# Performance work log

Measured on AMD Instinct MI355X. Metric: run time of the kernel, lower is better.

## Reference

```python
import jax, jax.numpy as jnp
import numpy as np
import math

B = 8192       # batch (tokens)
HID = 4096     # hidden size
H = 32         # num query heads
KV = 8         # num kv heads
GQA = H // KV  # 4
D = 128        # head dim
RBIT = 128     # hash bits
QKV = (H + 2 * KV) * D  # 6144


def setup_inputs() -> dict:
    key = jax.random.key(0)
    k1, k2, k3 = jax.random.split(key, 3)
    hidden = jax.random.normal(k1, (B, HID), jnp.float32)
    proj_w = jax.random.normal(k2, (HID, QKV), jnp.float32) * 0.02
    proj_b = jnp.zeros((QKV,), jnp.float32)
    # xavier_uniform init for hash weight [D, RBIT]
    limit = math.sqrt(6.0 / (D + RBIT))
    hash_w = jax.random.uniform(k3, (D, RBIT), jnp.float32, -limit, limit)
    return {"hidden": hidden, "proj_w": proj_w, "proj_b": proj_b, "hash_w": hash_w}


def reference(hidden, proj_w, proj_b, hash_w):
    # fused qkv projection
    qkv = hidden @ proj_w + proj_b                     # [B, QKV]
    q = qkv[:, : H * D].reshape(B, H, D)               # [B, H, D]
    k = qkv[:, H * D : (H + KV) * D].reshape(B, KV, 1, D)
    k = jnp.broadcast_to(k, (B, KV, GQA, D)).reshape(B, H, D)  # GQA expand

    inv_sqrt_d = 1.0 / math.sqrt(D)
    attn_weights = jnp.einsum("bhd,bhd->bh", q, k) * inv_sqrt_d  # with_norm=True

    # hash codes: BinaryStochastic (training mode): (tanh(x)+1)/2
    q_code = (jnp.tanh(q @ hash_w) + 1.0) * 0.5        # [B, H, RBIT]
    k_code = (jnp.tanh(k @ hash_w) + 1.0) * 0.5
    ham_dist = jnp.abs(q_code - k_code).sum(axis=-1)   # [B, H]
    ham_weights = 1.0 - 2.0 * ham_dist / RBIT

    # with_norm: scale by |q| |k| / sqrt(D)
    q_norm = jnp.linalg.norm(q, axis=-1)
    k_norm = jnp.linalg.norm(k, axis=-1)
    ham_weights = ham_weights * q_norm * k_norm * inv_sqrt_d

    return attn_weights.reshape(-1), ham_weights.reshape(-1)
```

## Files before the change

### kernel.cpp

```cpp
#include <hip/hip_runtime.h>
#include <hip/hip_bf16.h>
#include <cstdint>
#include <cstddef>

#define B_TOK 8192
#define HID   4096
#define NH    32
#define NKV   8
#define DH    128
#define RB    128
#define KDIM  4096
#define NOUT  5120
#define QKVW  6144

typedef __bf16 bf16x8 __attribute__((ext_vector_type(8)));
typedef __bf16 bf16x4 __attribute__((ext_vector_type(4)));
typedef float  f32x4  __attribute__((ext_vector_type(4)));

__device__ __forceinline__ void async_ld16(const void* g, void* l) {
  __builtin_amdgcn_global_load_lds(
      (__attribute__((address_space(1))) void*)(g),
      (__attribute__((address_space(3))) void*)(l), 16, 0, 0);
}

__device__ __forceinline__ float code_of(float x) {
  const float e = exp2f(x * -2.885390081777927f);
  return __builtin_amdgcn_rcpf(1.0f + e);
}


#define NB_HID  16384
#define NB_WT   5120
#define NB_HASH 64

__global__ void prep_kernel(const float* __restrict__ hidden, __bf16* __restrict__ Abf,
                            const float* __restrict__ W, __bf16* __restrict__ Wt,
                            const float* __restrict__ hw, __bf16* __restrict__ hwT) {
  __shared__ float t[64][65];
  const int bx  = blockIdx.x;
  const int tid = threadIdx.x;

  if (bx < NB_HID) {
    const int i = bx * 256 + tid;
    const float4 v0 = ((const float4*)hidden)[2 * i];
    const float4 v1 = ((const float4*)hidden)[2 * i + 1];
    bf16x8 o;
    o[0] = (__bf16)v0.x; o[1] = (__bf16)v0.y; o[2] = (__bf16)v0.z; o[3] = (__bf16)v0.w;
    o[4] = (__bf16)v1.x; o[5] = (__bf16)v1.y; o[6] = (__bf16)v1.z; o[7] = (__bf16)v1.w;
    ((bf16x8*)Abf)[i] = o;
  } else if (bx < NB_HID + NB_WT) {
    const int bt = bx - NB_HID;
    const int n0 = (bt % 80) * 64;
    const int k0 = (bt / 80) * 64;
    const int c4 = tid & 15;
    const int rr = tid >> 4;
#pragma unroll
    for (int j = 0; j < 4; ++j) {
      const int r = rr + j * 16;
      const float4 v = *(const float4*)&W[(size_t)(k0 + r) * QKVW + n0 + c4 * 4];
      t[r][c4 * 4 + 0] = v.x; t[r][c4 * 4 + 1] = v.y;
      t[r][c4 * 4 + 2] = v.z; t[r][c4 * 4 + 3] = v.w;
    }
    __syncthreads();
    const int c8 = tid & 7;
    const int nn = tid >> 3;
#pragma unroll
    for (int jj = 0; jj < 2; ++jj) {
      const int n = nn + jj * 32;
      bf16x8 o;
#pragma unroll
      for (int i = 0; i < 8; ++i) o[i] = (__bf16)t[c8 * 8 + i][n];
      *(bf16x8*)&Wt[(size_t)(n0 + n) * KDIM + k0 + c8 * 8] = o;
    }
  } else {
    const int idx = (bx - NB_HID - NB_WT) * 256 + tid;
    const int r = idx >> 7;
    const int d = idx & 127;
    hwT[r * RB + d] = (__bf16)hw[(size_t)d * RB + r];
  }
}


#define BK    32
#define KT    (KDIM / BK)
#define SLOT  24576

__global__ __launch_bounds__(256, 2) void gemm_qk(const __bf16* __restrict__ A,
                                                  const __bf16* __restrict__ Bt,
                                                  const float* __restrict__ bias,
                                                  __bf16* __restrict__ C) {
  __shared__ __align__(1024) char smem[3 * SLOT];

  const int tid  = threadIdx.x;
  const int lane = tid & 63;
  const int wave = tid >> 6;
  const int wm   = wave >> 1;
  const int wn   = wave & 1;

  const int lin = blockIdx.x;
  const int xcd = lin & 7;
  const int seq = lin >> 3;
  const int m0  = (xcd * 8 + (seq & 7)) * 128;
  const int n0  = (seq >> 3) * 256;

  const int srow = tid >> 2;
  const int sxk  = ((tid & 3) ^ ((tid >> 3) & 3)) * 8;
  const __bf16* ga = A  + (size_t)(m0 + srow) * KDIM + sxk;
  const __bf16* gb = Bt + (size_t)(n0 + srow) * KDIM + sxk;
  const int ldsA = wave * 1024;

#define STAGE(koff, sl) do {                                        \
    const __bf16* ga_ = ga + (koff);                                \
    const __bf16* gb_ = gb + (koff);                                \
    async_ld16(ga_,              (sl) + ldsA);                      \
    async_ld16(ga_ +  64 * KDIM, (sl) + 4096  + ldsA);              \
    async_ld16(gb_,              (sl) + 8192  + ldsA);              \
    async_ld16(gb_ +  64 * KDIM, (sl) + 12288 + ldsA);              \
    async_ld16(gb_ + 128 * KDIM, (sl) + 16384 + ldsA);              \
    async_ld16(gb_ + 192 * KDIM, (sl) + 20480 + ldsA);              \
  } while (0)

  const int fr = lane & 15;
  const int xc = (lane >> 4) ^ ((fr >> 1) & 3);
  const int aoff = (wm * 64 + fr) * 64 + xc * 16;
  const int boff = (wn * 128 + fr) * 64 + xc * 16;

  f32x4 acc[4][8] = {};

#define COMPUTE(sl) do {                                                          \
    bf16x8 af[4]; bf16x8 bfv[8];                                                  \
    _Pragma("unroll")                                                             \
    for (int mi = 0; mi < 4; ++mi)                                                \
      af[mi] = *(const bf16x8*)((sl) + aoff + mi * 1024);                         \
    _Pragma("unroll")                                                             \
    for (int ni = 0; ni < 8; ++ni)                                                \
      bfv[ni] = *(const bf16x8*)((sl) + 8192 + boff + ni * 1024);                 \
    __builtin_amdgcn_s_setprio(1);                                                \
    _Pragma("unroll")                                                             \
    for (int mi = 0; mi < 4; ++mi)                                                \
      _Pragma("unroll")                                                           \
      for (int ni = 0; ni < 8; ++ni)                                              \
        acc[mi][ni] = __builtin_amdgcn_mfma_f32_16x16x32_bf16(af[mi], bfv[ni],    \
                                                              acc[mi][ni], 0, 0, 0); \
    __builtin_amdgcn_s_setprio(0);                                                \
  } while (0)

  char* s0 = smem;
  char* s1 = smem + SLOT;
  char* s2 = smem + 2 * SLOT;

  STAGE(0, s0);
  STAGE(BK, s1);

  for (int t = 0; t < KT - 1; ++t) {
    asm volatile("s_waitcnt vmcnt(6)" ::: "memory");
    __builtin_amdgcn_s_barrier();
    __builtin_amdgcn_sched_barrier(0);
    if (t < KT - 2) STAGE((t + 2) * BK, s2);
    COMPUTE(s0);
    char* tmp = s0; s0 = s1; s1 = s2; s2 = tmp;
  }
  asm volatile("s_waitcnt vmcnt(0)" ::: "memory");
  __builtin_amdgcn_s_barrier();
  __builtin_amdgcn_sched_barrier(0);
  COMPUTE(s0);

#undef STAGE
#undef COMPUTE

  const int cl = lane & 15;
  const int rq = (lane >> 4) * 4;
#pragma unroll
  for (int ni = 0; ni < 8; ++ni) {
    const int gn = n0 + wn * 128 + ni * 16 + cl;
    const float bb = bias[gn];
#pragma unroll
    for (int mi = 0; mi < 4; ++mi) {
      const int gm = m0 + wm * 64 + mi * 16 + rq;
#pragma unroll
      for (int r = 0; r < 4; ++r)
        C[(size_t)(gm + r) * NOUT + gn] = (__bf16)(acc[mi][ni][r] + bb);
    }
  }
}


__global__ void phase2_kernel(const __bf16* __restrict__ QK,
                              const __bf16* __restrict__ hwT,
                              float* __restrict__ out) {
  __shared__ __bf16 As[48][136];
  __shared__ float code[40][132];
  __shared__ float rednorm[40];
  __shared__ float reddot[32];

  const int tid  = threadIdx.x;
  const int lane = tid & 63;
  const int wave = tid >> 6;
  const int b = blockIdx.x;

  const __bf16* src = QK + (size_t)b * NOUT;
  for (int i = tid; i < 640; i += 256) {
    const int row = i >> 4;
    const int col = (i & 15) * 8;
    *(uint4*)(&As[row][col]) = *(const uint4*)(src + i * 8);
  }

  const int fr = lane & 15;
  const int fk = (lane >> 4) * 8;
  bf16x8 bf[2][4];
#pragma unroll
  for (int nn = 0; nn < 2; ++nn) {
    const int ni = wave + nn * 4;
#pragma unroll
    for (int ks = 0; ks < 4; ++ks)
      bf[nn][ks] = *(const bf16x8*)(hwT + (size_t)(ni * 16 + fr) * RB + ks * 32 + fk);
  }
  __syncthreads();

#pragma unroll
  for (int mi = 0; mi < 3; ++mi) {
    bf16x8 af[4];
#pragma unroll
    for (int ks = 0; ks < 4; ++ks)
      af[ks] = *(const bf16x8*)(&As[mi * 16 + fr][ks * 32 + fk]);
#pragma unroll
    for (int nn = 0; nn < 2; ++nn) {
      const int ni = wave + nn * 4;
      f32x4 acc = {0.f, 0.f, 0.f, 0.f};
#pragma unroll
      for (int ks = 0; ks < 4; ++ks)
        acc = __builtin_amdgcn_mfma_f32_16x16x32_bf16(af[ks], bf[nn][ks], acc, 0, 0, 0);
      const int row0 = mi * 16 + (lane >> 4) * 4;
      const int col  = ni * 16 + (lane & 15);
#pragma unroll
      for (int r = 0; r < 4; ++r) {
        const int row = row0 + r;
        if (row < 40) code[row][col] = code_of(acc[r]);
      }
    }
  }

  {
    const int q = lane >> 4;
    const int c = lane & 15;
    const int ti = (wave == 1 || wave == 3) ? 1 : 0;
    const int tj = (wave >= 2) ? 2 : ti;
    bf16x8 fa[4], fb[4];
#pragma unroll
    for (int ks = 0; ks < 4; ++ks) {
      fa[ks] = *(const bf16x8*)(&As[ti * 16 + fr][ks * 32 + fk]);
      fb[ks] = *(const bf16x8*)(&As[tj * 16 + fr][ks * 32 + fk]);
    }
    f32x4 g = {0.f, 0.f, 0.f, 0.f};
#pragma unroll
    for (int ks = 0; ks < 4; ++ks)
      g = __builtin_amdgcn_mfma_f32_16x16x32_bf16(fa[ks], fb[ks], g, 0, 0, 0);
    if (ti == tj) {
      if ((c >> 2) == q) rednorm[ti * 16 + c] = g[c & 3];
    } else {
      if (c == ti * 4 + q) {
#pragma unroll
        for (int r = 0; r < 4; ++r) reddot[ti * 16 + q * 4 + r] = g[r];
      }
    }
    if (wave == 0) {
      bf16x8 fc[4];
#pragma unroll
      for (int ks = 0; ks < 4; ++ks)
        fc[ks] = *(const bf16x8*)(&As[32 + fr][ks * 32 + fk]);
      f32x4 g2 = {0.f, 0.f, 0.f, 0.f};
#pragma unroll
      for (int ks = 0; ks < 4; ++ks)
        g2 = __builtin_amdgcn_mfma_f32_16x16x32_bf16(fc[ks], fc[ks], g2, 0, 0, 0);
      if ((c >> 2) == q && c < 8) rednorm[32 + c] = g2[c & 3];
    }
  }
  __syncthreads();

  const int h   = tid >> 3;
  const int sub = tid & 7;
  const int kr  = 32 + (h >> 2);
  float s = 0.f;
#pragma unroll
  for (int j = 0; j < 16; ++j) {
    const int c = sub + 8 * j;
    s += fabsf(code[h][c] - code[kr][c]);
  }
  s += __shfl_down(s, 4, 8);
  s += __shfl_down(s, 2, 8);
  s += __shfl_down(s, 1, 8);
  if (sub == 0) {
    const float invsq = 0.08838834764831843f;
    out[(size_t)b * NH + h] = reddot[h] * invsq;
    const float hamw = (1.0f - s * (1.0f / 64.0f)) *
                       sqrtf(rednorm[h]) * sqrtf(rednorm[kr]) * invsq;
    out[(size_t)(B_TOK * NH) + (size_t)b * NH + h] = hamw;
  }
}


extern "C" void kernel_launch(void* const* d_in, const int* in_sizes, int n_in,
                              void* d_out, int out_size, void* d_ws, size_t ws_size,
                              hipStream_t stream) {
  const float* hidden = (const float*)d_in[0];
  const float* proj_w = (const float*)d_in[1];
  const float* proj_b = (const float*)d_in[2];
  const float* hash_w = (const float*)d_in[3];
  float* out = (float*)d_out;

  char* w = (char*)d_ws;
  __bf16* Abf = (__bf16*)(w);
  __bf16* Wt  = (__bf16*)(w + 67108864);
  __bf16* QK  = (__bf16*)(w + 67108864 + 41943040);
  __bf16* hwT = (__bf16*)(w + 67108864 + 41943040 + 83886080);

  prep_kernel<<<NB_HID + NB_WT + NB_HASH, 256, 0, stream>>>(hidden, Abf, proj_w, Wt,
                                                            hash_w, hwT);
  gemm_qk<<<1280, 256, 0, stream>>>(Abf, Wt, proj_b, QK);
  phase2_kernel<<<B_TOK, 256, 0, stream>>>(QK, hwT, out);
}
```

Baseline: 608.3 us.

## Double-buffer MFMA fragments in registers to overlap LDS reads with compute

Restructures the GEMM main loop so the LDS fragments for the next k-tile are loaded into a second register set while MFMAs run on the current one, with the loop unrolled by two to alternate buffers. The aim is to hide LDS read latency behind matrix-core work. In exchange it doubles fragment register usage, which may reduce occupancy. It also changes the global-load wait from vmcnt(6) to vmcnt(0), so less global prefetch overlaps each barrier.

```diff
diff --git a/kernel.cpp b/kernel.cpp
--- a/kernel.cpp
+++ b/kernel.cpp
@@ -126,47 +126,62 @@
   const int boff = (wn * 128 + fr) * 64 + xc * 16;
 
   f32x4 acc[4][8] = {};
-
-#define COMPUTE(sl) do {                                                          \
-    bf16x8 af[4]; bf16x8 bfv[8];                                                  \
+  bf16x8 afX[4], bfX[8], afY[4], bfY[8];
+
+  char* s0 = smem;
+  char* s1 = smem + SLOT;
+  char* s2 = smem + 2 * SLOT;
+
+#define BODY(tt, CA, CB, NA, NB, DO_STAGE) do {                                   \
+    asm volatile("s_waitcnt vmcnt(0)" ::: "memory");                              \
+    __builtin_amdgcn_s_barrier();                                                 \
+    __builtin_amdgcn_sched_barrier(0);                                            \
+    if (DO_STAGE) STAGE(((tt) + 2) * BK, s2);                                     \
     _Pragma("unroll")                                                             \
     for (int mi = 0; mi < 4; ++mi)                                                \
-      af[mi] = *(const bf16x8*)((sl) + aoff + mi * 1024);                         \
+      NA[mi] = *(const bf16x8*)(s1 + aoff + mi * 1024);                           \
     _Pragma("unroll")                                                             \
     for (int ni = 0; ni < 8; ++ni)                                                \
-      bfv[ni] = *(const bf16x8*)((sl) + 8192 + boff + ni * 1024);                 \
+      NB[ni] = *(const bf16x8*)(s1 + 8192 + boff + ni * 1024);                    \
     __builtin_amdgcn_s_setprio(1);                                                \
     _Pragma("unroll")                                                             \
     for (int mi = 0; mi < 4; ++mi)                                                \
       _Pragma("unroll")                                                           \
       for (int ni = 0; ni < 8; ++ni)                                              \
-        acc[mi][ni] = __builtin_amdgcn_mfma_f32_16x16x32_bf16(af[mi], bfv[ni],    \
+        acc[mi][ni] = __builtin_amdgcn_mfma_f32_16x16x32_bf16(CA[mi], CB[ni],     \
                                                               acc[mi][ni], 0, 0, 0); \
     __builtin_amdgcn_s_setprio(0);                                                \
+    { char* tmp_ = s0; s0 = s1; s1 = s2; s2 = tmp_; }                             \
   } while (0)
-
-  char* s0 = smem;
-  char* s1 = smem + SLOT;
-  char* s2 = smem + 2 * SLOT;
 
   STAGE(0, s0);
   STAGE(BK, s1);
-
-  for (int t = 0; t < KT - 1; ++t) {
-    asm volatile("s_waitcnt vmcnt(6)" ::: "memory");
-    __builtin_amdgcn_s_barrier();
-    __builtin_amdgcn_sched_barrier(0);
-    if (t < KT - 2) STAGE((t + 2) * BK, s2);
-    COMPUTE(s0);
-    char* tmp = s0; s0 = s1; s1 = s2; s2 = tmp;
-  }
-  asm volatile("s_waitcnt vmcnt(0)" ::: "memory");
+  asm volatile("s_waitcnt vmcnt(6)" ::: "memory");
   __builtin_amdgcn_s_barrier();
   __builtin_amdgcn_sched_barrier(0);
-  COMPUTE(s0);
+#pragma unroll
+  for (int mi = 0; mi < 4; ++mi)
+    afX[mi] = *(const bf16x8*)(s0 + aoff + mi * 1024);
+#pragma unroll
+  for (int ni = 0; ni < 8; ++ni)
+    bfX[ni] = *(const bf16x8*)(s0 + 8192 + boff + ni * 1024);
+
+  for (int t = 0; t < KT - 2; t += 2) {
+    BODY(t,     afX, bfX, afY, bfY, true);
+    BODY(t + 1, afY, bfY, afX, bfX, true);
+  }
+  BODY(KT - 2, afX, bfX, afY, bfY, false);
+  __builtin_amdgcn_s_setprio(1);
+#pragma unroll
+  for (int mi = 0; mi < 4; ++mi)
+#pragma unroll
+    for (int ni = 0; ni < 8; ++ni)
+      acc[mi][ni] = __builtin_amdgcn_mfma_f32_16x16x32_bf16(afY[mi], bfY[ni],
+                                                            acc[mi][ni], 0, 0, 0);
+  __builtin_amdgcn_s_setprio(0);
 
 #undef STAGE
-#undef COMPUTE
+#undef BODY
 
   const int cl = lane & 15;
   const int rq = (lane >> 4) * 4;
```

After: 627.3 us. 1.03x slower.
